# Performance work log

Measured on AMD Instinct MI355X. Metric: run time of the kernel, lower is better.

The kernel has to match this reference:

```python
import jax, jax.numpy as jnp
import numpy as np

N, E, D, H, C, G = 50000, 800000, 128, 128, 16, 512


def setup_inputs() -> dict:
    key = jax.random.key(0)
    ks = jax.random.split(key, 8)

    def glorot(k, shape):
        lim = float(np.sqrt(6.0 / (shape[0] + shape[1])))
        return jax.random.uniform(k, shape, jnp.float32, -lim, lim)

    x = jax.random.normal(ks[0], (N, D), jnp.float32)
    edge_index = jax.random.randint(ks[1], (2, E), 0, N, dtype=jnp.int32)
    batch = jnp.sort(jax.random.randint(ks[2], (N,), 0, G, dtype=jnp.int32))
    return {
        'x': x,
        'edge_index': edge_index,
        'batch': batch,
        'W1': glorot(ks[3], (D, H)), 'b1': jnp.zeros((H,), jnp.float32),
        'W2': glorot(ks[4], (H, H)), 'b2': jnp.zeros((H,), jnp.float32),
        'lW1': glorot(ks[5], (4 * H, 2 * H)), 'lb1': jnp.zeros((2 * H,), jnp.float32),
        'lW2': glorot(ks[6], (2 * H, C)), 'lb2': jnp.zeros((C,), jnp.float32),
    }


def _gcn_norm(edge_index, n):
    # add self loops, then symmetric normalization D^-1/2 (A+I) D^-1/2
    loop = jnp.arange(n, dtype=edge_index.dtype)
    src = jnp.concatenate([edge_index[0], loop])
    dst = jnp.concatenate([edge_index[1], loop])
    ones = jnp.ones(src.shape[0], jnp.float32)
    deg = jax.ops.segment_sum(ones, dst, num_segments=n)
    dis = jnp.where(deg > 0, jax.lax.rsqrt(jnp.maximum(deg, 1.0)), 0.0)
    norm = dis[src] * dis[dst]  # [E+N]
    return src, dst, norm


def _gcn_conv(x, src, dst, norm, W, b, n):
    h = x @ W                                   # [N, H] transform first (PyG order)
    msg = h[src] * norm[:, None]                # gather + normalize, [E+N, H]
    out = jax.ops.segment_sum(msg, dst, num_segments=n)  # scatter-add
    return out + b


def _pool(x, batch, g):
    cnt = jax.ops.segment_sum(jnp.ones(x.shape[0], x.dtype), batch, num_segments=g)
    mean = jax.ops.segment_sum(x, batch, num_segments=g) / jnp.maximum(cnt, 1.0)[:, None]
    mx = jax.ops.segment_max(x, batch, num_segments=g)
    mx = jnp.where(cnt[:, None] > 0, mx, 0.0)
    return mean, mx


def reference(x, edge_index, batch, W1, b1, W2, b2, lW1, lb1, lW2, lb2):
    n = x.shape[0]
    src, dst, norm = _gcn_norm(edge_index, n)
    x0 = jax.nn.relu(_gcn_conv(x, src, dst, norm, W1, b1, n))   # dropout=identity (eval)
    g0_mean, g0_max = _pool(x0, batch, G)
    x1 = jax.nn.relu(_gcn_conv(x0, src, dst, norm, W2, b2, n))
    g1_mean, g1_max = _pool(x1, batch, G)
    g = jnp.concatenate([g0_mean, g0_max, g1_mean, g1_max], axis=-1)  # [G, 4H]
    h = jax.nn.relu(g @ lW1 + lb1)
    return h @ lW2 + lb2  # [G, C]
```

## Files before the change

### kernel.cpp

```cpp
#include <hip/hip_runtime.h>
#include <hip/hip_bf16.h>

#define NN 50000
#define EE 800000
#define DD 128
#define HH 128
#define CC 16
#define GG 512
#define NBLK_SCAN 196
#define NPAD 50176
#define GEMM_BLOCKS 782
#define FILL_BLOCKS 3125
#define POOLF (4 * GG * HH + GG)

typedef __attribute__((ext_vector_type(8))) short short8v;
typedef __attribute__((ext_vector_type(8))) unsigned short ushort8v;
typedef __attribute__((ext_vector_type(4))) float f32x4;

__device__ inline unsigned short f2bf(float x) {
    unsigned int u = __float_as_uint(x);
    u += 0x7fffu + ((u >> 16) & 1u);
    return (unsigned short)(u >> 16);
}

__global__ __launch_bounds__(256) void k_init(const float* __restrict__ W1, const float* __restrict__ W2,
                                              unsigned short* __restrict__ Wf,
                                              int* __restrict__ deg, float* __restrict__ pools) {
    int tid = blockIdx.x * 256 + threadIdx.x;
    int nt = gridDim.x * 256;
    for (int i = tid; i < NPAD; i += nt) deg[i] = 0;
    for (int i = tid; i < POOLF; i += nt) pools[i] = 0.0f;
    for (int idx = tid; idx < 4096; idx += nt) {
        const float* W = (idx >> 11) ? W2 : W1;
        int id2 = idx & 2047;
        int lane = id2 & 63, ct = (id2 >> 6) & 7, kt = id2 >> 9;
        int col = ct * 16 + (lane & 15);
        int k0 = kt * 32 + (lane >> 4) * 8;
        ushort8v v;
        #pragma unroll
        for (int j = 0; j < 8; ++j) v[j] = f2bf(W[(k0 + j) * 128 + col]);
        *(ushort8v*)(Wf + idx * 8) = v;
    }
}

__global__ __launch_bounds__(256) void k_deg(const int* __restrict__ ei, int* __restrict__ deg) {
    int e = blockIdx.x * 256 + threadIdx.x;
    if (e < EE) atomicAdd(&deg[ei[EE + e]], 1);
}

__global__ __launch_bounds__(256) void k_scan1(const int* __restrict__ deg,
                                               int* __restrict__ offs, int* __restrict__ bsum,
                                               float* __restrict__ dis) {
    __shared__ int tmp[256];
    int i = blockIdx.x * 256 + threadIdx.x;
    int v = (i < NN) ? deg[i] : 0;
    if (i < NN) dis[i] = rsqrtf((float)v + 1.0f);
    tmp[threadIdx.x] = v;
    __syncthreads();
    for (int off = 1; off < 256; off <<= 1) {
        int t = (threadIdx.x >= off) ? tmp[threadIdx.x - off] : 0;
        __syncthreads();
        tmp[threadIdx.x] += t;
        __syncthreads();
    }
    if (i < NN) offs[i] = tmp[threadIdx.x] - v;
    if (threadIdx.x == 255) bsum[blockIdx.x] = tmp[255];
}

__global__ __launch_bounds__(256) void k_scan23(int* __restrict__ offs, const int* __restrict__ bsum,
                                                int* __restrict__ cursor) {
    __shared__ int sdata[256];
    int t = threadIdx.x;
    sdata[t] = (t < (int)blockIdx.x && t < NBLK_SCAN) ? bsum[t] : 0;
    __syncthreads();
    for (int off = 128; off > 0; off >>= 1) {
        if (t < off) sdata[t] += sdata[t + off];
        __syncthreads();
    }
    int base = sdata[0];
    int i = blockIdx.x * 256 + t;
    if (i < NN) {
        int v = offs[i] + base;
        offs[i] = v;
        cursor[i] = v;
    }
}

__global__ __launch_bounds__(256) void k_fillgemm(const float* __restrict__ Af,
                                                  const unsigned short* __restrict__ Wf,
                                                  unsigned short* __restrict__ O,
                                                  const int* __restrict__ ei,
                                                  const float* __restrict__ dis,
                                                  int* __restrict__ cursor,
                                                  unsigned int* __restrict__ adj) {
    __shared__ unsigned short Wl[16384];
    if (blockIdx.x < GEMM_BLOCKS) {
        #pragma unroll
        for (int idx = threadIdx.x; idx < 2048; idx += 256)
            *(ushort8v*)(Wl + idx * 8) = *(const ushort8v*)(Wf + idx * 8);
        __syncthreads();

        int wid = threadIdx.x >> 6, lane = threadIdx.x & 63;
        int b = lane >> 4;
        int row = blockIdx.x * 64 + wid * 16 + (lane & 15);
        int r = min(row, NN - 1);
        const float* ap = Af + (size_t)r * 128 + b * 8;
        short8v a[4];
        #pragma unroll
        for (int kt = 0; kt < 4; ++kt) {
            float4 f0 = *(const float4*)(ap + kt * 32);
            float4 f1 = *(const float4*)(ap + kt * 32 + 4);
            short8v v;
            v[0] = (short)f2bf(f0.x); v[1] = (short)f2bf(f0.y);
            v[2] = (short)f2bf(f0.z); v[3] = (short)f2bf(f0.w);
            v[4] = (short)f2bf(f1.x); v[5] = (short)f2bf(f1.y);
            v[6] = (short)f2bf(f1.z); v[7] = (short)f2bf(f1.w);
            a[kt] = v;
        }
        f32x4 z = 0.0f;
        f32x4 acc[8] = {z, z, z, z, z, z, z, z};
        #pragma unroll
        for (int kt = 0; kt < 4; ++kt) {
            #pragma unroll
            for (int ct = 0; ct < 8; ++ct) {
                short8v bfrag = *(const short8v*)(Wl + ((kt * 8 + ct) * 64 + lane) * 8);
                acc[ct] = __builtin_amdgcn_mfma_f32_16x16x32_bf16(a[kt], bfrag, acc[ct], 0, 0, 0);
            }
        }
        int orow = blockIdx.x * 64 + wid * 16 + b * 4;
        unsigned short* op = O + (size_t)orow * 128 + (lane & 15);
        #pragma unroll
        for (int j = 0; j < 4; ++j) {
            #pragma unroll
            for (int ct = 0; ct < 8; ++ct)
                op[(size_t)j * 128 + ct * 16] = f2bf(acc[ct][j]);
        }
    } else {
        int e = (blockIdx.x - GEMM_BLOCKS) * 256 + threadIdx.x;
        if (e < EE) {
            int s = ei[e];
            int d = ei[EE + e];
            float nrm = dis[s] * dis[d];
            int pos = atomicAdd(&cursor[d], 1);
            adj[pos] = ((unsigned int)s << 16) | (unsigned int)f2bf(nrm);
        }
    }
}

__global__ __launch_bounds__(256) void k_gemm(const unsigned short* __restrict__ Ab,
                                              const unsigned short* __restrict__ Wf,
                                              unsigned short* __restrict__ O) {
    __shared__ unsigned short Wl[16384];
    #pragma unroll
    for (int idx = threadIdx.x; idx < 2048; idx += 256)
        *(ushort8v*)(Wl + idx * 8) = *(const ushort8v*)(Wf + idx * 8);
    __syncthreads();

    int wid = threadIdx.x >> 6, lane = threadIdx.x & 63;
    int b = lane >> 4;
    int row = blockIdx.x * 64 + wid * 16 + (lane & 15);
    const unsigned short* ap = Ab + (size_t)row * 128 + b * 8;
    short8v a[4];
    #pragma unroll
    for (int kt = 0; kt < 4; ++kt) a[kt] = *(const short8v*)(ap + kt * 32);

    f32x4 z = 0.0f;
    f32x4 acc[8] = {z, z, z, z, z, z, z, z};
    #pragma unroll
    for (int kt = 0; kt < 4; ++kt) {
        #pragma unroll
        for (int ct = 0; ct < 8; ++ct) {
            short8v bfrag = *(const short8v*)(Wl + ((kt * 8 + ct) * 64 + lane) * 8);
            acc[ct] = __builtin_amdgcn_mfma_f32_16x16x32_bf16(a[kt], bfrag, acc[ct], 0, 0, 0);
        }
    }
    int orow = blockIdx.x * 64 + wid * 16 + b * 4;
    unsigned short* op = O + (size_t)orow * 128 + (lane & 15);
    #pragma unroll
    for (int j = 0; j < 4; ++j) {
        #pragma unroll
        for (int ct = 0; ct < 8; ++ct)
            op[(size_t)j * 128 + ct * 16] = f2bf(acc[ct][j]);
    }
}

__global__ __launch_bounds__(256) void k_conv(const unsigned short* __restrict__ h,
                                              const unsigned int* __restrict__ adj,
                                              const int* __restrict__ row_start,
                                              const int* __restrict__ deg,
                                              const float* __restrict__ dis,
                                              const float* __restrict__ bias,
                                              const int* __restrict__ batch,
                                              unsigned short* __restrict__ xout,
                                              float* __restrict__ gsum,
                                              float* __restrict__ gmax,
                                              float* __restrict__ cnt,
                                              int flags) {
    __shared__ float lacc[16][128];
    __shared__ int lb[16];
    const int tid = threadIdx.x;
    const int wid = tid >> 6, lane = tid & 63;
    const int g = lane >> 4, l = lane & 15;
    const int nrow = wid * 4 + g;
    const int node = blockIdx.x * 16 + nrow;
    const int fb = l * 8;

    const float di = dis[node];
    const float d2 = di * di;
    const uint4 hv = *(const uint4*)(h + (size_t)node * 128 + fb);
    const float4 bv0 = *(const float4*)(bias + fb);
    const float4 bv1 = *(const float4*)(bias + fb + 4);
    float acc[8];
    acc[0] = __uint_as_float(hv.x << 16)         * d2 + bv0.x;
    acc[1] = __uint_as_float(hv.x & 0xffff0000u) * d2 + bv0.y;
    acc[2] = __uint_as_float(hv.y << 16)         * d2 + bv0.z;
    acc[3] = __uint_as_float(hv.y & 0xffff0000u) * d2 + bv0.w;
    acc[4] = __uint_as_float(hv.z << 16)         * d2 + bv1.x;
    acc[5] = __uint_as_float(hv.z & 0xffff0000u) * d2 + bv1.y;
    acc[6] = __uint_as_float(hv.w << 16)         * d2 + bv1.z;
    acc[7] = __uint_as_float(hv.w & 0xffff0000u) * d2 + bv1.w;

    const int rs = row_start[node];
    const int n  = deg[node];
    const unsigned int* ap = adj + rs;
    const int sl = lane & 48;
    const int nfull = n & ~15;

    for (int k = 0; k < nfull; k += 16) {
        unsigned int e = ap[k + l];
        #pragma unroll
        for (int j = 0; j < 16; ++j) {
            unsigned int ej = __shfl(e, sl + j);
            float w = __uint_as_float(ej << 16);
            const uint4 v = *(const uint4*)(h + (size_t)(ej >> 16) * 128 + fb);
            acc[0] = fmaf(__uint_as_float(v.x << 16),         w, acc[0]);
            acc[1] = fmaf(__uint_as_float(v.x & 0xffff0000u), w, acc[1]);
            acc[2] = fmaf(__uint_as_float(v.y << 16),         w, acc[2]);
            acc[3] = fmaf(__uint_as_float(v.y & 0xffff0000u), w, acc[3]);
            acc[4] = fmaf(__uint_as_float(v.z << 16),         w, acc[4]);
            acc[5] = fmaf(__uint_as_float(v.z & 0xffff0000u), w, acc[5]);
            acc[6] = fmaf(__uint_as_float(v.w << 16),         w, acc[6]);
            acc[7] = fmaf(__uint_as_float(v.w & 0xffff0000u), w, acc[7]);
        }
    }
    if (nfull < n) {
        unsigned int e = ap[min(nfull + l, n - 1)];
        #pragma unroll
        for (int j = 0; j < 16; ++j) {
            unsigned int ej = __shfl(e, sl + j);
            float w = (nfull + j < n) ? __uint_as_float(ej << 16) : 0.0f;
            const uint4 v = *(const uint4*)(h + (size_t)(ej >> 16) * 128 + fb);
            acc[0] = fmaf(__uint_as_float(v.x << 16),         w, acc[0]);
            acc[1] = fmaf(__uint_as_float(v.x & 0xffff0000u), w, acc[1]);
            acc[2] = fmaf(__uint_as_float(v.y << 16),         w, acc[2]);
            acc[3] = fmaf(__uint_as_float(v.y & 0xffff0000u), w, acc[3]);
            acc[4] = fmaf(__uint_as_float(v.z << 16),         w, acc[4]);
            acc[5] = fmaf(__uint_as_float(v.z & 0xffff0000u), w, acc[5]);
            acc[6] = fmaf(__uint_as_float(v.w << 16),         w, acc[6]);
            acc[7] = fmaf(__uint_as_float(v.w & 0xffff0000u), w, acc[7]);
        }
    }
    #pragma unroll
    for (int p = 0; p < 8; ++p) acc[p] = fmaxf(acc[p], 0.0f);

    if (flags & 1) {
        uint4 o;
        o.x = (unsigned)f2bf(acc[0]) | ((unsigned)f2bf(acc[1]) << 16);
        o.y = (unsigned)f2bf(acc[2]) | ((unsigned)f2bf(acc[3]) << 16);
        o.z = (unsigned)f2bf(acc[4]) | ((unsigned)f2bf(acc[5]) << 16);
        o.w = (unsigned)f2bf(acc[6]) | ((unsigned)f2bf(acc[7]) << 16);
        *(uint4*)(xout + (size_t)node * 128 + fb) = o;
    }

    #pragma unroll
    for (int p = 0; p < 8; ++p) lacc[nrow][fb + p] = acc[p];
    if (l == 0) lb[nrow] = batch[node];
    __syncthreads();
    {
        const int f = tid & 127;
        const bool domax = tid >= 128;
        float s = lacc[0][f];
        int cur = lb[0], run = 1;
        #pragma unroll
        for (int w = 1; w < 16; ++w) {
            float a = lacc[w][f];
            if (lb[w] == cur) {
                s = domax ? fmaxf(s, a) : (s + a);
                ++run;
            } else {
                if (domax) {
                    atomicMax((int*)&gmax[cur * 128 + f], __float_as_int(s));
                } else {
                    atomicAdd(&gsum[cur * 128 + f], s);
                    if (f == 0 && (flags & 2)) atomicAdd(cnt + cur, (float)run);
                }
                s = a; cur = lb[w]; run = 1;
            }
        }
        if (domax) {
            atomicMax((int*)&gmax[cur * 128 + f], __float_as_int(s));
        } else {
            atomicAdd(&gsum[cur * 128 + f], s);
            if (f == 0 && (flags & 2)) atomicAdd(cnt + cur, (float)run);
        }
    }
}

__global__ __launch_bounds__(256) void k_mlp(const float* __restrict__ gsum0,
                                             const float* __restrict__ gmax0,
                                             const float* __restrict__ gsum1,
                                             const float* __restrict__ gmax1,
                                             const float* __restrict__ cnt,
                                             const float* __restrict__ lW1,
                                             const float* __restrict__ lb1,
                                             const float* __restrict__ lW2,
                                             const float* __restrict__ lb2,
                                             float* __restrict__ out) {
    __shared__ float gl[512];
    __shared__ float hb[256];
    __shared__ float part[256];
    int r = blockIdx.x;
    float inv = 1.0f / fmaxf(cnt[r], 1.0f);
    for (int k = threadIdx.x; k < 512; k += 256) {
        int seg = k >> 7, f = k & 127;
        float v;
        if (seg == 0)      v = gsum0[r * 128 + f] * inv;
        else if (seg == 1) v = gmax0[r * 128 + f];
        else if (seg == 2) v = gsum1[r * 128 + f] * inv;
        else               v = gmax1[r * 128 + f];
        gl[k] = v;
    }
    __syncthreads();
    {
        int j = threadIdx.x;
        float acc = lb1[j];
        for (int k = 0; k < 512; ++k) acc += gl[k] * lW1[k * 256 + j];
        hb[j] = fmaxf(acc, 0.f);
    }
    __syncthreads();
    {
        int c = threadIdx.x & 15, ch = threadIdx.x >> 4;
        float p = 0.f;
        #pragma unroll
        for (int j2 = 0; j2 < 16; ++j2) p += hb[ch * 16 + j2] * lW2[(ch * 16 + j2) * 16 + c];
        part[threadIdx.x] = p;
    }
    __syncthreads();
    if (threadIdx.x < 16) {
        float s = lb2[threadIdx.x];
        #pragma unroll
        for (int ch2 = 0; ch2 < 16; ++ch2) s += part[ch2 * 16 + threadIdx.x];
        out[r * 16 + threadIdx.x] = s;
    }
}

extern "C" void kernel_launch(void* const* d_in, const int* in_sizes, int n_in,
                              void* d_out, int out_size, void* d_ws, size_t ws_size,
                              hipStream_t stream) {
    const float* x    = (const float*)d_in[0];
    const int*   ei   = (const int*)d_in[1];
    const int*   batch= (const int*)d_in[2];
    const float* W1   = (const float*)d_in[3];
    const float* b1   = (const float*)d_in[4];
    const float* W2   = (const float*)d_in[5];
    const float* b2   = (const float*)d_in[6];
    const float* lW1  = (const float*)d_in[7];
    const float* lb1  = (const float*)d_in[8];
    const float* lW2  = (const float*)d_in[9];
    const float* lb2  = (const float*)d_in[10];
    float* out = (float*)d_out;

    unsigned short* hbuf = (unsigned short*)d_ws;
    unsigned short* x0b  = hbuf + (size_t)NPAD * 128;
    unsigned short* wf   = x0b + (size_t)NPAD * 128;
    float* dis   = (float*)(wf + 32768);
    float* gsum0 = dis + NPAD;
    float* gmax0 = gsum0 + GG * HH;
    float* gsum1 = gmax0 + GG * HH;
    float* gmax1 = gsum1 + GG * HH;
    float* cnt   = gmax1 + GG * HH;
    int*   deg    = (int*)(cnt + GG);
    int*   offs   = deg + NPAD;
    int*   cursor = offs + NPAD;
    int*   bsum   = cursor + NPAD;
    unsigned int* adj = (unsigned int*)(bsum + 256);

    k_init<<<256, 256, 0, stream>>>(W1, W2, wf, deg, gsum0);

    k_deg<<<(EE + 255) / 256, 256, 0, stream>>>(ei, deg);
    k_scan1<<<NBLK_SCAN, 256, 0, stream>>>(deg, offs, bsum, dis);
    k_scan23<<<NBLK_SCAN, 256, 0, stream>>>(offs, bsum, cursor);

    k_fillgemm<<<GEMM_BLOCKS + FILL_BLOCKS, 256, 0, stream>>>(x, wf, hbuf, ei, dis, cursor, adj);

    k_conv<<<NN / 16, 256, 0, stream>>>(hbuf, adj, offs, deg, dis, b1, batch,
                                        x0b, gsum0, gmax0, cnt, 3);
    k_gemm<<<GEMM_BLOCKS, 256, 0, stream>>>(x0b, wf + 16384, hbuf);
    k_conv<<<NN / 16, 256, 0, stream>>>(hbuf, adj, offs, deg, dis, b2, batch,
                                        x0b, gsum1, gmax1, cnt, 0);

    k_mlp<<<GG, 256, 0, stream>>>(gsum0, gmax0, gsum1, gmax1, cnt, lW1, lb1, lW2, lb2, out);
}
```

Before: 205.1 us.

## Fuse second GEMM into first conv epilogue and prescale rows by degree norm

Folds the source-side D^-1/2 factor into the GEMM output rows and applies the destination factor once at the end of aggregation, so adjacency entries store only a 16-bit source index instead of a packed index plus bf16 weight. The layer-2 GEMM is fused into the layer-1 conv epilogue using the relu'd tile held in shared memory, removing the separate GEMM kernel and the x0 round trip. W is read from global memory instead of being staged in LDS in the first GEMM. The gather loop becomes plain adds, at the cost of extra work and register pressure inside the conv kernel.

```diff
diff --git a/kernel.cpp b/kernel.cpp
--- a/kernel.cpp
+++ b/kernel.cpp
@@ -88,18 +88,12 @@
 
 __global__ __launch_bounds__(256) void k_fillgemm(const float* __restrict__ Af,
                                                   const unsigned short* __restrict__ Wf,
+                                                  const float* __restrict__ dis,
                                                   unsigned short* __restrict__ O,
                                                   const int* __restrict__ ei,
-                                                  const float* __restrict__ dis,
                                                   int* __restrict__ cursor,
-                                                  unsigned int* __restrict__ adj) {
-    __shared__ unsigned short Wl[16384];
+                                                  unsigned short* __restrict__ adj16) {
     if (blockIdx.x < GEMM_BLOCKS) {
-        #pragma unroll
-        for (int idx = threadIdx.x; idx < 2048; idx += 256)
-            *(ushort8v*)(Wl + idx * 8) = *(const ushort8v*)(Wf + idx * 8);
-        __syncthreads();
-
         int wid = threadIdx.x >> 6, lane = threadIdx.x & 63;
         int b = lane >> 4;
         int row = blockIdx.x * 64 + wid * 16 + (lane & 15);
@@ -123,7 +117,7 @@
         for (int kt = 0; kt < 4; ++kt) {
             #pragma unroll
             for (int ct = 0; ct < 8; ++ct) {
-                short8v bfrag = *(const short8v*)(Wl + ((kt * 8 + ct) * 64 + lane) * 8);
+                short8v bfrag = *(const short8v*)(Wf + ((kt * 8 + ct) * 64 + lane) * 8);
                 acc[ct] = __builtin_amdgcn_mfma_f32_16x16x32_bf16(a[kt], bfrag, acc[ct], 0, 0, 0);
             }
         }
@@ -131,73 +125,38 @@
         unsigned short* op = O + (size_t)orow * 128 + (lane & 15);
         #pragma unroll
         for (int j = 0; j < 4; ++j) {
+            float dr = dis[orow + j];
             #pragma unroll
             for (int ct = 0; ct < 8; ++ct)
-                op[(size_t)j * 128 + ct * 16] = f2bf(acc[ct][j]);
+                op[(size_t)j * 128 + ct * 16] = f2bf(acc[ct][j] * dr);
         }
     } else {
         int e = (blockIdx.x - GEMM_BLOCKS) * 256 + threadIdx.x;
         if (e < EE) {
             int s = ei[e];
             int d = ei[EE + e];
-            float nrm = dis[s] * dis[d];
             int pos = atomicAdd(&cursor[d], 1);
-            adj[pos] = ((unsigned int)s << 16) | (unsigned int)f2bf(nrm);
-        }
-    }
-}
-
-__global__ __launch_bounds__(256) void k_gemm(const unsigned short* __restrict__ Ab,
-                                              const unsigned short* __restrict__ Wf,
-                                              unsigned short* __restrict__ O) {
-    __shared__ unsigned short Wl[16384];
-    #pragma unroll
-    for (int idx = threadIdx.x; idx < 2048; idx += 256)
-        *(ushort8v*)(Wl + idx * 8) = *(const ushort8v*)(Wf + idx * 8);
-    __syncthreads();
-
-    int wid = threadIdx.x >> 6, lane = threadIdx.x & 63;
-    int b = lane >> 4;
-    int row = blockIdx.x * 64 + wid * 16 + (lane & 15);
-    const unsigned short* ap = Ab + (size_t)row * 128 + b * 8;
-    short8v a[4];
-    #pragma unroll
-    for (int kt = 0; kt < 4; ++kt) a[kt] = *(const short8v*)(ap + kt * 32);
-
-    f32x4 z = 0.0f;
-    f32x4 acc[8] = {z, z, z, z, z, z, z, z};
-    #pragma unroll
-    for (int kt = 0; kt < 4; ++kt) {
-        #pragma unroll
-        for (int ct = 0; ct < 8; ++ct) {
-            short8v bfrag = *(const short8v*)(Wl + ((kt * 8 + ct) * 64 + lane) * 8);
-            acc[ct] = __builtin_amdgcn_mfma_f32_16x16x32_bf16(a[kt], bfrag, acc[ct], 0, 0, 0);
-        }
-    }
-    int orow = blockIdx.x * 64 + wid * 16 + b * 4;
-    unsigned short* op = O + (size_t)orow * 128 + (lane & 15);
-    #pragma unroll
-    for (int j = 0; j < 4; ++j) {
-        #pragma unroll
-        for (int ct = 0; ct < 8; ++ct)
-            op[(size_t)j * 128 + ct * 16] = f2bf(acc[ct][j]);
+            adj16[pos] = (unsigned short)s;
+        }
     }
 }
 
 __global__ __launch_bounds__(256) void k_conv(const unsigned short* __restrict__ h,
-                                              const unsigned int* __restrict__ adj,
+                                              const unsigned short* __restrict__ adj16,
                                               const int* __restrict__ row_start,
                                               const int* __restrict__ deg,
                                               const float* __restrict__ dis,
                                               const float* __restrict__ bias,
                                               const int* __restrict__ batch,
-                                              unsigned short* __restrict__ xout,
+                                              const unsigned short* __restrict__ W2f,
+                                              unsigned short* __restrict__ h2out,
                                               float* __restrict__ gsum,
                                               float* __restrict__ gmax,
                                               float* __restrict__ cnt,
                                               int flags) {
-    __shared__ float lacc[16][128];
+    __shared__ float lacc[16][132];
     __shared__ int lb[16];
+    __shared__ float sdis[16];
     const int tid = threadIdx.x;
     const int wid = tid >> 6, lane = tid & 63;
     const int g = lane >> 4, l = lane & 15;
@@ -206,33 +165,48 @@
     const int fb = l * 8;
 
     const float di = dis[node];
-    const float d2 = di * di;
     const uint4 hv = *(const uint4*)(h + (size_t)node * 128 + fb);
     const float4 bv0 = *(const float4*)(bias + fb);
     const float4 bv1 = *(const float4*)(bias + fb + 4);
     float acc[8];
-    acc[0] = __uint_as_float(hv.x << 16)         * d2 + bv0.x;
-    acc[1] = __uint_as_float(hv.x & 0xffff0000u) * d2 + bv0.y;
-    acc[2] = __uint_as_float(hv.y << 16)         * d2 + bv0.z;
-    acc[3] = __uint_as_float(hv.y & 0xffff0000u) * d2 + bv0.w;
-    acc[4] = __uint_as_float(hv.z << 16)         * d2 + bv1.x;
-    acc[5] = __uint_as_float(hv.z & 0xffff0000u) * d2 + bv1.y;
-    acc[6] = __uint_as_float(hv.w << 16)         * d2 + bv1.z;
-    acc[7] = __uint_as_float(hv.w & 0xffff0000u) * d2 + bv1.w;
+    acc[0] = __uint_as_float(hv.x << 16);
+    acc[1] = __uint_as_float(hv.x & 0xffff0000u);
+    acc[2] = __uint_as_float(hv.y << 16);
+    acc[3] = __uint_as_float(hv.y & 0xffff0000u);
+    acc[4] = __uint_as_float(hv.z << 16);
+    acc[5] = __uint_as_float(hv.z & 0xffff0000u);
+    acc[6] = __uint_as_float(hv.w << 16);
+    acc[7] = __uint_as_float(hv.w & 0xffff0000u);
 
     const int rs = row_start[node];
     const int n  = deg[node];
-    const unsigned int* ap = adj + rs;
+    const unsigned short* ap = adj16 + rs;
     const int sl = lane & 48;
     const int nfull = n & ~15;
 
     for (int k = 0; k < nfull; k += 16) {
-        unsigned int e = ap[k + l];
+        int e = ap[k + l];
         #pragma unroll
         for (int j = 0; j < 16; ++j) {
-            unsigned int ej = __shfl(e, sl + j);
-            float w = __uint_as_float(ej << 16);
-            const uint4 v = *(const uint4*)(h + (size_t)(ej >> 16) * 128 + fb);
+            int ej = __shfl(e, sl + j);
+            const uint4 v = *(const uint4*)(h + (size_t)ej * 128 + fb);
+            acc[0] += __uint_as_float(v.x << 16);
+            acc[1] += __uint_as_float(v.x & 0xffff0000u);
+            acc[2] += __uint_as_float(v.y << 16);
+            acc[3] += __uint_as_float(v.y & 0xffff0000u);
+            acc[4] += __uint_as_float(v.z << 16);
+            acc[5] += __uint_as_float(v.z & 0xffff0000u);
+            acc[6] += __uint_as_float(v.w << 16);
+            acc[7] += __uint_as_float(v.w & 0xffff0000u);
+        }
+    }
+    if (nfull < n) {
+        int e = ap[min(nfull + l, n - 1)];
+        #pragma unroll
+        for (int j = 0; j < 16; ++j) {
+            int ej = __shfl(e, sl + j);
+            float w = (nfull + j < n) ? 1.0f : 0.0f;
+            const uint4 v = *(const uint4*)(h + (size_t)ej * 128 + fb);
             acc[0] = fmaf(__uint_as_float(v.x << 16),         w, acc[0]);
             acc[1] = fmaf(__uint_as_float(v.x & 0xffff0000u), w, acc[1]);
             acc[2] = fmaf(__uint_as_float(v.y << 16),         w, acc[2]);
@@ -243,39 +217,16 @@
             acc[7] = fmaf(__uint_as_float(v.w & 0xffff0000u), w, acc[7]);
         }
     }
-    if (nfull < n) {
-        unsigned int e = ap[min(nfull + l, n - 1)];
-        #pragma unroll
-        for (int j = 0; j < 16; ++j) {
-            unsigned int ej = __shfl(e, sl + j);
-            float w = (nfull + j < n) ? __uint_as_float(ej << 16) : 0.0f;
-            const uint4 v = *(const uint4*)(h + (size_t)(ej >> 16) * 128 + fb);
-            acc[0] = fmaf(__uint_as_float(v.x << 16),         w, acc[0]);
-            acc[1] = fmaf(__uint_as_float(v.x & 0xffff0000u), w, acc[1]);
-            acc[2] = fmaf(__uint_as_float(v.y << 16),         w, acc[2]);
-            acc[3] = fmaf(__uint_as_float(v.y & 0xffff0000u), w, acc[3]);
-            acc[4] = fmaf(__uint_as_float(v.z << 16),         w, acc[4]);
-            acc[5] = fmaf(__uint_as_float(v.z & 0xffff0000u), w, acc[5]);
-            acc[6] = fmaf(__uint_as_float(v.w << 16),         w, acc[6]);
-            acc[7] = fmaf(__uint_as_float(v.w & 0xffff0000u), w, acc[7]);
-        }
-    }
+    float bvv[8] = {bv0.x, bv0.y, bv0.z, bv0.w, bv1.x, bv1.y, bv1.z, bv1.w};
     #pragma unroll
-    for (int p = 0; p < 8; ++p) acc[p] = fmaxf(acc[p], 0.0f);
-
-    if (flags & 1) {
-        uint4 o;
-        o.x = (unsigned)f2bf(acc[0]) | ((unsigned)f2bf(acc[1]) << 16);
-        o.y = (unsigned)f2bf(acc[2]) | ((unsigned)f2bf(acc[3]) << 16);
-        o.z = (unsigned)f2bf(acc[4]) | ((unsigned)f2bf(acc[5]) << 16);
-        o.w = (unsigned)f2bf(acc[6]) | ((unsigned)f2bf(acc[7]) << 16);
-        *(uint4*)(xout + (size_t)node * 128 + fb) = o;
-    }
-
-    #pragma unroll
-    for (int p = 0; p < 8; ++p) lacc[nrow][fb + p] = acc[p];
+    for (int p = 0; p < 8; ++p) {
+        float v = fmaxf(fmaf(di, acc[p], bvv[p]), 0.0f);
+        lacc[nrow][fb + p] = v;
+    }
     if (l == 0) lb[nrow] = batch[node];
-    __syncthreads();
+    if (tid < 16) sdis[tid] = dis[blockIdx.x * 16 + tid];
+    __syncthreads();
+
     {
         const int f = tid & 127;
         const bool domax = tid >= 128;
@@ -302,6 +253,35 @@
         } else {
             atomicAdd(&gsum[cur * 128 + f], s);
             if (f == 0 && (flags & 2)) atomicAdd(cnt + cur, (float)run);
+        }
+    }
+
+    if (flags & 4) {
+        const int ct0 = wid * 2, ct1 = wid * 2 + 1;
+        f32x4 c0 = 0.0f, c1 = 0.0f;
+        #pragma unroll
+        for (int kt = 0; kt < 4; ++kt) {
+            const float* arow = &lacc[lane & 15][kt * 32 + (lane >> 4) * 8];
+            float4 fa = *(const float4*)arow;
+            float4 fc = *(const float4*)(arow + 4);
+            short8v af;
+            af[0] = (short)f2bf(fa.x); af[1] = (short)f2bf(fa.y);
+            af[2] = (short)f2bf(fa.z); af[3] = (short)f2bf(fa.w);
+            af[4] = (short)f2bf(fc.x); af[5] = (short)f2bf(fc.y);
+            af[6] = (short)f2bf(fc.z); af[7] = (short)f2bf(fc.w);
+            short8v b0 = *(const short8v*)(W2f + ((kt * 8 + ct0) * 64 + lane) * 8);
+            short8v b1 = *(const short8v*)(W2f + ((kt * 8 + ct1) * 64 + lane) * 8);
+            c0 = __builtin_amdgcn_mfma_f32_16x16x32_bf16(af, b0, c0, 0, 0, 0);
+            c1 = __builtin_amdgcn_mfma_f32_16x16x32_bf16(af, b1, c1, 0, 0, 0);
+        }
+        const int node0 = blockIdx.x * 16;
+        #pragma unroll
+        for (int j = 0; j < 4; ++j) {
+            int r = (lane >> 4) * 4 + j;
+            float dr = sdis[r];
+            unsigned short* op = h2out + (size_t)(node0 + r) * 128 + (lane & 15);
+            op[ct0 * 16] = f2bf(c0[j] * dr);
+            op[ct1 * 16] = f2bf(c1[j] * dr);
         }
     }
 }
@@ -371,8 +351,8 @@
     float* out = (float*)d_out;
 
     unsigned short* hbuf = (unsigned short*)d_ws;
-    unsigned short* x0b  = hbuf + (size_t)NPAD * 128;
-    unsigned short* wf   = x0b + (size_t)NPAD * 128;
+    unsigned short* h2b  = hbuf + (size_t)NPAD * 128;
+    unsigned short* wf   = h2b + (size_t)NPAD * 128;
     float* dis   = (float*)(wf + 32768);
     float* gsum0 = dis + NPAD;
     float* gmax0 = gsum0 + GG * HH;
@@ -383,7 +363,7 @@
     int*   offs   = deg + NPAD;
     int*   cursor = offs + NPAD;
     int*   bsum   = cursor + NPAD;
-    unsigned int* adj = (unsigned int*)(bsum + 256);
+    unsigned short* adj16 = (unsigned short*)(bsum + 256);
 
     k_init<<<256, 256, 0, stream>>>(W1, W2, wf, deg, gsum0);
 
@@ -391,13 +371,13 @@
     k_scan1<<<NBLK_SCAN, 256, 0, stream>>>(deg, offs, bsum, dis);
     k_scan23<<<NBLK_SCAN, 256, 0, stream>>>(offs, bsum, cursor);
 
-    k_fillgemm<<<GEMM_BLOCKS + FILL_BLOCKS, 256, 0, stream>>>(x, wf, hbuf, ei, dis, cursor, adj);
-
-    k_conv<<<NN / 16, 256, 0, stream>>>(hbuf, adj, offs, deg, dis, b1, batch,
-                                        x0b, gsum0, gmax0, cnt, 3);
-    k_gemm<<<GEMM_BLOCKS, 256, 0, stream>>>(x0b, wf + 16384, hbuf);
-    k_conv<<<NN / 16, 256, 0, stream>>>(hbuf, adj, offs, deg, dis, b2, batch,
-                                        x0b, gsum1, gmax1, cnt, 0);
+    k_fillgemm<<<GEMM_BLOCKS + FILL_BLOCKS, 256, 0, stream>>>(x, wf, dis, hbuf, ei, cursor, adj16);
+
+    k_conv<<<NN / 16, 256, 0, stream>>>(hbuf, adj16, offs, deg, dis, b1, batch,
+                                        wf + 16384, h2b, gsum0, gmax0, cnt, 2 | 4);
+    k_conv<<<NN / 16, 256, 0, stream>>>(h2b, adj16, offs, deg, dis, b2, batch,
+                                        (const unsigned short*)nullptr, (unsigned short*)nullptr,
+                                        gsum1, gmax1, cnt, 0);
 
     k_mlp<<<GG, 256, 0, stream>>>(gsum0, gmax0, gsum1, gmax1, cnt, lW1, lb1, lW2, lb2, out);
 }
```

Result: slower. 234.4 us (+14.3%).
